# Performance work log

Measured on AMD Instinct MI355X. Metric: run time of the kernel, lower is better.

Reference implementation:

```python
import math
import jax, jax.numpy as jnp
import numpy as np

N_HEAD = 16

def _slopes(n_head):
    # Matches MHA_aLiBi.get_slope (static, so computed with numpy)
    cp2 = 2 ** int(math.floor(math.log2(n_head)))
    slopes = (0.5) ** np.arange(1, cp2 + 1)
    if cp2 < n_head:
        intra = 1.0 / math.sqrt(2.0)
        pair = intra ** np.arange(1, 1 + 2 * (n_head - cp2), 2)
        slopes = np.sort(np.concatenate([slopes, pair]))[::-1]
    return jnp.asarray(slopes, dtype=jnp.float32)  # [H]

def _alibi_bias(S):
    # bias[i,j] = -(i-j) for i>=j, 0 for i<j
    d = jnp.arange(S)[:, None] - jnp.arange(S)[None, :]
    return -jnp.maximum(d, 0).astype(jnp.float32)  # [S,S]

def setup_inputs() -> dict:
    key = jax.random.key(0)
    B, S, D = 2, 2048, 1024
    ks = jax.random.split(key, 12)
    f = lambda k, sh: jax.random.normal(k, sh, dtype=jnp.float32)
    inp = {
        "q": f(ks[0], (B, S, D)),
        "k": f(ks[1], (B, S, D)),
        "v": f(ks[2], (B, S, D)),
        "mask": jnp.tril(jnp.ones((S, S), dtype=jnp.int32))[None, None],  # causal [1,1,S,S]
        "wq_w": f(ks[3], (D, D)) * 0.02, "wq_b": f(ks[4], (D,)) * 0.02,
        "wk_w": f(ks[5], (D, D)) * 0.02, "wk_b": f(ks[6], (D,)) * 0.02,
        "wv_w": f(ks[7], (D, D)) * 0.02, "wv_b": f(ks[8], (D,)) * 0.02,
        "out_w": f(ks[9], (D, D)) * 0.02, "out_b": f(ks[10], (D,)) * 0.02,
    }
    return inp

def reference(q, k, v, mask, wq_w, wq_b, wk_w, wk_b, wv_w, wv_b, out_w, out_b):
    B, S, D = q.shape
    H = N_HEAD
    hd = D // H
    lin = lambda x, w, b: x @ w.T + b  # torch nn.Linear
    # project and split heads: [B,S,D] -> [B,H,S,hd]
    split = lambda x: x.reshape(B, S, H, hd).transpose(0, 2, 1, 3)
    wq = split(lin(q, wq_w, wq_b))
    wk = split(lin(k, wk_w, wk_b))
    wv = split(lin(v, wv_w, wv_b))
    qk = jnp.einsum("bhsd,bhtd->bhst", wq, wk)  # [B,H,S,S] (no 1/sqrt(d) scaling, per source)
    alibi = _alibi_bias(S)[None, :, :] * _slopes(H)[:, None, None]  # [H,S,S]
    attn = qk + alibi[None]
    attn = jnp.where(mask == 0, jnp.float32(-1e9), attn)
    attn = jax.nn.softmax(attn, axis=-1)
    out = jnp.einsum("bhst,bhtd->bhsd", attn, wv)
    out = out.transpose(0, 2, 1, 3).reshape(B, S, D)
    return lin(out, out_w, out_b)
```

## Files before the change

kernel.cpp:

```cpp
#include <hip/hip_runtime.h>
#include <hip/hip_bf16.h>
#include <cstdint>
#include <cstddef>

#define DEV static __device__ __forceinline__

typedef float f32x4 __attribute__((ext_vector_type(4)));
typedef __bf16 bf16x8 __attribute__((ext_vector_type(8)));
typedef __bf16 bf16x4 __attribute__((ext_vector_type(4)));

#define EXP2F(x) __builtin_amdgcn_exp2f(x)

union B8 {
  uint4 u4;
  uint32_t u[4];
  unsigned short s[8];
  bf16x8 v;
};
union B4 {
  uint2 u2;
  unsigned short s[4];
  bf16x4 v;
};

DEV unsigned short bfbits(float x) {
  union { __bf16 h; unsigned short s; } z; z.h = (__bf16)x; return z.s;
}
DEV uint32_t pk2(float x, float y) {
  union { __bf16 h[2]; uint32_t u; } z;
  z.h[0] = (__bf16)x; z.h[1] = (__bf16)y; return z.u;
}

DEV f32x4 mfma_bf16(bf16x8 a, bf16x8 b, f32x4 c) {
  return __builtin_amdgcn_mfma_f32_16x16x32_bf16(a, b, c, 0, 0, 0);
}

DEV void gload16(const void* g, void* l) {
  __builtin_amdgcn_global_load_lds(
      (const __attribute__((address_space(1))) void*)g,
      (__attribute__((address_space(3))) void*)l, 16, 0, 0);
}

__global__ __launch_bounds__(256)
void cvt_all(const float* __restrict__ q, const float* __restrict__ k,
             const float* __restrict__ v,
             const float* __restrict__ wq, const float* __restrict__ wk,
             const float* __restrict__ wv, const float* __restrict__ ow,
             unsigned short* __restrict__ dst) {
  const int bid = blockIdx.x;
  const size_t base = ((size_t)bid << 11) + ((size_t)threadIdx.x << 3);
  const float* src;
  size_t rel;
  if (bid < 2048)      { src = q; rel = base; }
  else if (bid < 4096) { src = k; rel = base - (1u << 22); }
  else if (bid < 6144) { src = v; rel = base - (2u << 22); }
  else {
    const int wseg = (bid - 6144) >> 9;
    src = wseg == 0 ? wq : wseg == 1 ? wk : wseg == 2 ? wv : ow;
    rel = base & 1048575u;
  }
  float4 a0 = *(const float4*)(src + rel);
  float4 a1 = *(const float4*)(src + rel + 4);
  B8 p;
  p.u[0] = pk2(a0.x, a0.y); p.u[1] = pk2(a0.z, a0.w);
  p.u[2] = pk2(a1.x, a1.y); p.u[3] = pk2(a1.z, a1.w);
  *(uint4*)(dst + base) = p.u4;
}

__global__ __launch_bounds__(256, 2)
void gemm_qkv_b(const unsigned short* __restrict__ qb,
                const unsigned short* __restrict__ kb,
                const unsigned short* __restrict__ vb,
                const unsigned short* __restrict__ wqb,
                const unsigned short* __restrict__ wkb,
                const unsigned short* __restrict__ wvb,
                const float* __restrict__ bq, const float* __restrict__ bk,
                const float* __restrict__ bv,
                unsigned short* __restrict__ Qp, unsigned short* __restrict__ Kp,
                unsigned short* __restrict__ Vt) {
  const int K = 1024, N = 1024;
  __shared__ __align__(16) unsigned short As[64 * 64];
  __shared__ __align__(16) unsigned short Bs[128 * 64];
  const int bid = blockIdx.x;
  const int lbid = (bid & 7) * 192 + (bid >> 3);
  const int proj = lbid >> 9;
  const int t = lbid & 511;
  const int mb = t >> 3, nb = t & 7;
  const unsigned short* A  = proj == 0 ? qb  : proj == 1 ? kb  : vb;
  const unsigned short* Bw = proj == 0 ? wqb : proj == 1 ? wkb : wvb;
  const float* bias        = proj == 0 ? bq  : proj == 1 ? bk  : bv;
  const int tid = threadIdx.x;
  const int lane = tid & 63, w = tid >> 6;
  const int qc = lane & 15, g = lane >> 4;
  f32x4 acc[4][2] = {};

  const int lrow = lane >> 3, lg = lane & 7;
  const int gsrc = lg ^ lrow;
  const unsigned short* ag = A  + (size_t)(mb * 64 + w * 16 + lrow) * K + gsrc * 8;
  const unsigned short* bg = Bw + (size_t)(nb * 128 + w * 32 + lrow) * K + gsrc * 8;
  unsigned short* al = &As[(w * 16) * 64];
  unsigned short* bl = &Bs[(w * 32) * 64];

  for (int kt = 0; kt < 16; ++kt) {
    __syncthreads();
#pragma unroll
    for (int i = 0; i < 2; ++i)
      gload16(ag + i * (8 * 1024) + kt * 64, al + (i * 8) * 64);
#pragma unroll
    for (int i = 0; i < 4; ++i)
      gload16(bg + i * (8 * 1024) + kt * 64, bl + (i * 8) * 64);
    __syncthreads();

    B8 af[4][2], bfr[2][2];
#pragma unroll
    for (int mi = 0; mi < 4; ++mi)
#pragma unroll
      for (int kk = 0; kk < 2; ++kk) {
        const int row = mi * 16 + qc;
        const int slot = ((kk << 2) + g) ^ (row & 7);
        af[mi][kk].u4 = *(const uint4*)&As[(row << 6) + (slot << 3)];
      }
#pragma unroll
    for (int ni = 0; ni < 2; ++ni)
#pragma unroll
      for (int kk = 0; kk < 2; ++kk) {
        const int row = w * 32 + ni * 16 + qc;
        const int slot = ((kk << 2) + g) ^ (row & 7);
        bfr[ni][kk].u4 = *(const uint4*)&Bs[(row << 6) + (slot << 3)];
      }
#pragma unroll
    for (int kk = 0; kk < 2; ++kk)
#pragma unroll
      for (int mi = 0; mi < 4; ++mi)
#pragma unroll
        for (int ni = 0; ni < 2; ++ni)
          acc[mi][ni] = mfma_bf16(af[mi][kk].v, bfr[ni][kk].v, acc[mi][ni]);
  }

  unsigned short* Cv = proj == 0 ? Qp : proj == 1 ? Kp : Vt;
  const bool vt_mode = (proj == 2);
#pragma unroll
  for (int ni = 0; ni < 2; ++ni) {
    const int col = nb * 128 + w * 32 + ni * 16 + qc;
    const float bv = bias[col];
#pragma unroll
    for (int mi = 0; mi < 4; ++mi) {
#pragma unroll
      for (int r = 0; r < 4; ++r) {
        const int row = mb * 64 + mi * 16 + g * 4 + r;
        const float val = acc[mi][ni][r] + bv;
        if (!vt_mode) {
          Cv[(size_t)row * N + col] = bfbits(val);
        } else {
          const int b = row >> 11, ss = row & 2047, hh = col >> 6, d = col & 63;
          Cv[((size_t)((b * 16 + hh) * 64 + d) << 11) + ss] = bfbits(val);
        }
      }
    }
  }
}

__global__ __launch_bounds__(256, 2)
void gemm_out_b(const unsigned short* __restrict__ At,
                const unsigned short* __restrict__ wob,
                const float* __restrict__ bias, float* __restrict__ Cv) {
  const int K = 1024, N = 1024;
  __shared__ __align__(16) unsigned short As[64 * 64];
  __shared__ __align__(16) unsigned short Bs[128 * 64];
  const int bid = blockIdx.x;
  const int lbid = (bid & 7) * 64 + (bid >> 3);
  const int mb = lbid >> 3, nb = lbid & 7;
  const int tid = threadIdx.x;
  const int lane = tid & 63, w = tid >> 6;
  const int qc = lane & 15, g = lane >> 4;
  f32x4 acc[4][2] = {};

  const int lrow = lane >> 3, lg = lane & 7;
  const int gsrc = lg ^ lrow;
  const unsigned short* ag = At  + (size_t)(mb * 64 + w * 16 + lrow) * K + gsrc * 8;
  const unsigned short* bg = wob + (size_t)(nb * 128 + w * 32 + lrow) * K + gsrc * 8;
  unsigned short* al = &As[(w * 16) * 64];
  unsigned short* bl = &Bs[(w * 32) * 64];

  for (int kt = 0; kt < 16; ++kt) {
    __syncthreads();
#pragma unroll
    for (int i = 0; i < 2; ++i)
      gload16(ag + i * (8 * 1024) + kt * 64, al + (i * 8) * 64);
#pragma unroll
    for (int i = 0; i < 4; ++i)
      gload16(bg + i * (8 * 1024) + kt * 64, bl + (i * 8) * 64);
    __syncthreads();

    B8 af[4][2], bfr[2][2];
#pragma unroll
    for (int mi = 0; mi < 4; ++mi)
#pragma unroll
      for (int kk = 0; kk < 2; ++kk) {
        const int row = mi * 16 + qc;
        const int slot = ((kk << 2) + g) ^ (row & 7);
        af[mi][kk].u4 = *(const uint4*)&As[(row << 6) + (slot << 3)];
      }
#pragma unroll
    for (int ni = 0; ni < 2; ++ni)
#pragma unroll
      for (int kk = 0; kk < 2; ++kk) {
        const int row = w * 32 + ni * 16 + qc;
        const int slot = ((kk << 2) + g) ^ (row & 7);
        bfr[ni][kk].u4 = *(const uint4*)&Bs[(row << 6) + (slot << 3)];
      }
#pragma unroll
    for (int kk = 0; kk < 2; ++kk)
#pragma unroll
      for (int mi = 0; mi < 4; ++mi)
#pragma unroll
        for (int ni = 0; ni < 2; ++ni)
          acc[mi][ni] = mfma_bf16(af[mi][kk].v, bfr[ni][kk].v, acc[mi][ni]);
  }

#pragma unroll
  for (int ni = 0; ni < 2; ++ni) {
    const int col = nb * 128 + w * 32 + ni * 16 + qc;
    const float bv = bias[col];
#pragma unroll
    for (int mi = 0; mi < 4; ++mi) {
#pragma unroll
      for (int r = 0; r < 4; ++r) {
        const int row = mb * 64 + mi * 16 + g * 4 + r;
        Cv[(size_t)row * N + col] = acc[mi][ni][r] + bv;
      }
    }
  }
}

__global__ __launch_bounds__(256, 4)
void flash_alibi(const unsigned short* __restrict__ Qp,
                 const unsigned short* __restrict__ Kp,
                 const unsigned short* __restrict__ Vt,
                 unsigned short* __restrict__ At) {
  const int S = 2048, Dm = 1024;
  const int bid0 = blockIdx.x;
  const int lbid = (bid0 & 7) * 128 + (bid0 >> 3);
  const int z = lbid >> 5, y = lbid & 31;
  const int s = ((8 * (y & 3)) + (y >> 2) + 8 * (z & 3) + (z >> 2)) & 31;
  const int h = z & 15, b = z >> 4;
  const int tid = threadIdx.x, lane = tid & 63, w = tid >> 6;
  const int qc = lane & 15, g = lane >> 4;
  const int q0 = s * 64 + w * 16;
  const int qcol = q0 + qc;
  const float slope = exp2f(-(float)(h + 1));
  const float L2E = 1.44269504f;
  const float ls1 = L2E * slope;
  const float THR = 11.54f;
  const size_t bS = (size_t)b * S;
  const int hoff = h * 64;
  const int ntile = s + 1;

  __shared__ __align__(16) unsigned short Ks[64 * 64];
  __shared__ __align__(16) unsigned short Vs[64 * 64];

  B8 qf[2];
  {
    const unsigned short* qa = Qp + (bS + qcol) * Dm + hoff + g * 8;
    qf[0].u4 = *(const uint4*)qa; qf[1].u4 = *(const uint4*)(qa + 32);
  }

  const int q7 = qc & 7;
  const int gk0 = g ^ q7;
  const int gk1 = gk0 ^ 4;
  const int krow = w * 16 + qc;
  const unsigned short* kgA = Kp + (bS + krow) * Dm + hoff + g * 8;
  const unsigned short* kgB = Kp + (bS + krow) * Dm + hoff + (g ^ 4) * 8;
  const unsigned short* vgA =
      Vt + (((size_t)((b * 16 + h) * 64 + krow)) << 11) + g * 8;
  const unsigned short* vgB =
      Vt + (((size_t)((b * 16 + h) * 64 + krow)) << 11) + (g ^ 4) * 8;
  unsigned short* kwA = &Ks[krow * 64 + gk0 * 8];
  unsigned short* kwB = &Ks[krow * 64 + gk1 * 8];
  unsigned short* vwA = &Vs[krow * 64 + gk0 * 8];
  unsigned short* vwB = &Vs[krow * 64 + gk1 * 8];
  uint4 krA, krB, vrA, vrB;

#define SLOAD(TT) do {                                                         \
    const size_t ko_ = ((size_t)(TT) << 6) * Dm;                               \
    krA = *(const uint4*)(kgA + ko_); krB = *(const uint4*)(kgB + ko_);        \
    vrA = *(const uint4*)(vgA + ((TT) << 6));                                  \
    vrB = *(const uint4*)(vgB + ((TT) << 6));                                  \
  } while (0)
#define SWRITE() do {                                                          \
    *(uint4*)kwA = krA; *(uint4*)kwB = krB;                                    \
    *(uint4*)vwA = vrA; *(uint4*)vwB = vrB;                                    \
  } while (0)

  const int sw = qc & 7;
  const unsigned short* krd0 = &Ks[qc * 64 + ((g ^ sw) << 3)];
  const unsigned short* krd1 = &Ks[qc * 64 + (((g ^ sw) ^ 4) << 3)];
  const unsigned short* vrd[4];
#pragma unroll
  for (int j = 0; j < 4; ++j)
    vrd[j] = &Vs[qc * 64 + ((((2 * j) + (g >> 1)) ^ sw) << 3) + (g & 1) * 4];

  f32x4 acc[4] = {};
  float m_run = 0.f, l_run = 0.f;
  const float abq = slope * (float)(g * 4 - qcol);

#define FRAGX(KV0, MASKED) do {                                                \
    const float kv0f = (float)(KV0);                                           \
    f32x4 sc_[4] = {};                                                         \
    _Pragma("unroll")                                                          \
    for (int f_ = 0; f_ < 4; ++f_) {                                           \
      B8 k0_, k1_;                                                             \
      k0_.u4 = *(const uint4*)(krd0 + f_ * 1024);                              \
      k1_.u4 = *(const uint4*)(krd1 + f_ * 1024);                              \
      sc_[f_] = mfma_bf16(k0_.v, qf[0].v, sc_[f_]);                            \
      sc_[f_] = mfma_bf16(k1_.v, qf[1].v, sc_[f_]);                            \
    }                                                                          \
    const float cb_ = (fmaf(slope, kv0f, abq) - m_run) * L2E;                  \
    float ein_[4][4]; float emax_ = -1e30f;                                    \
    _Pragma("unroll")                                                          \
    for (int f_ = 0; f_ < 4; ++f_) {                                           \
      const float cf_ = cb_ + (float)(16 * f_) * ls1;                          \
      _Pragma("unroll")                                                        \
      for (int r_ = 0; r_ < 4; ++r_) {                                         \
        float e_ = fmaf(sc_[f_][r_], L2E, cf_ + (float)r_ * ls1);              \
        if (MASKED) {                                                          \
          const int kv_ = (KV0) + f_ * 16 + g * 4 + r_;                        \
          if (kv_ > qcol) e_ = -1e30f;                                         \
        }                                                                      \
        ein_[f_][r_] = e_; emax_ = fmaxf(emax_, e_);                           \
      }                                                                        \
    }                                                                          \
    if (!__all(emax_ <= THR)) {                                                \
      float er_ = fmaxf(emax_, __shfl_xor(emax_, 16));                         \
      er_ = fmaxf(er_, __shfl_xor(er_, 32));                                   \
      er_ = fmaxf(er_, 0.f);                                                   \
      m_run += er_ * 0.69314718f;                                              \
      const float sfac_ = EXP2F(-er_);                                         \
      l_run *= sfac_;                                                          \
      _Pragma("unroll") for (int n_ = 0; n_ < 4; ++n_) acc[n_] = acc[n_] * sfac_; \
      _Pragma("unroll") for (int f_ = 0; f_ < 4; ++f_)                         \
        _Pragma("unroll") for (int r_ = 0; r_ < 4; ++r_) ein_[f_][r_] -= er_;  \
    }                                                                          \
    B8 pf0_, pf1_; float lsum_ = 0.f;                                          \
    _Pragma("unroll")                                                          \
    for (int f_ = 0; f_ < 4; ++f_) {                                           \
      _Pragma("unroll")                                                        \
      for (int r_ = 0; r_ < 4; ++r_) {                                         \
        const float p_ = EXP2F(ein_[f_][r_]);                                  \
        lsum_ += p_;                                                           \
        if (f_ == 0)      pf0_.v[r_]     = (__bf16)p_;                         \
        else if (f_ == 1) pf0_.v[4 + r_] = (__bf16)p_;                         \
        else if (f_ == 2) pf1_.v[r_]     = (__bf16)p_;                         \
        else              pf1_.v[4 + r_] = (__bf16)p_;                         \
      }                                                                        \
    }                                                                          \
    l_run += lsum_;                                                            \
    _Pragma("unroll")                                                          \
    for (int n_ = 0; n_ < 4; ++n_) {                                           \
      B8 v0_, v1_;                                                             \
      uint2 a0_ = *(const uint2*)(vrd[0] + n_ * 1024);                         \
      uint2 a1_ = *(const uint2*)(vrd[1] + n_ * 1024);                         \
      uint2 a2_ = *(const uint2*)(vrd[2] + n_ * 1024);                         \
      uint2 a3_ = *(const uint2*)(vrd[3] + n_ * 1024);                         \
      v0_.u[0] = a0_.x; v0_.u[1] = a0_.y;                                      \
      v0_.u[2] = a1_.x; v0_.u[3] = a1_.y;                                      \
      v1_.u[0] = a2_.x; v1_.u[1] = a2_.y;                                      \
      v1_.u[2] = a3_.x; v1_.u[3] = a3_.y;                                      \
      acc[n_] = mfma_bf16(v0_.v, pf0_.v, acc[n_]);                             \
      acc[n_] = mfma_bf16(v1_.v, pf1_.v, acc[n_]);                             \
    }                                                                          \
  } while (0)

  SLOAD(0);
  SWRITE();
  __syncthreads();

  for (int t = 0; t < ntile - 1; ++t) {
    SLOAD(t + 1);
    FRAGX(t << 6, 0);
    __syncthreads();
    SWRITE();
    __syncthreads();
  }
  FRAGX((ntile - 1) << 6, 1);

  float lt = l_run + __shfl_xor(l_run, 16);
  lt += __shfl_xor(lt, 32);
  const float ri = 1.0f / lt;
  unsigned short* ob = At + (bS + qcol) * Dm + hoff;
#pragma unroll
  for (int n = 0; n < 4; ++n) {
    B4 ov;
    ov.v[0] = (__bf16)(acc[n][0] * ri);
    ov.v[1] = (__bf16)(acc[n][1] * ri);
    ov.v[2] = (__bf16)(acc[n][2] * ri);
    ov.v[3] = (__bf16)(acc[n][3] * ri);
    *(uint2*)(ob + n * 16 + g * 4) = ov.u2;
  }
}

extern "C" void kernel_launch(void* const* d_in, const int* in_sizes, int n_in,
                              void* d_out, int out_size, void* d_ws, size_t ws_size,
                              hipStream_t stream) {
  const float* q    = (const float*)d_in[0];
  const float* k    = (const float*)d_in[1];
  const float* v    = (const float*)d_in[2];
  const float* wq_w = (const float*)d_in[4];
  const float* wq_b = (const float*)d_in[5];
  const float* wk_w = (const float*)d_in[6];
  const float* wk_b = (const float*)d_in[7];
  const float* wv_w = (const float*)d_in[8];
  const float* wv_b = (const float*)d_in[9];
  const float* ow   = (const float*)d_in[10];
  const float* ob   = (const float*)d_in[11];
  float* out = (float*)d_out;

  char* ws = (char*)d_ws;
  unsigned short* Qp = (unsigned short*)(ws);
  unsigned short* Kp = (unsigned short*)(ws + (8u << 20));
  unsigned short* Vt = (unsigned short*)(ws + (16u << 20));
  unsigned short* At = (unsigned short*)(ws + (24u << 20));
  unsigned short* cvt = (unsigned short*)(ws + (32u << 20));
  unsigned short* qb  = cvt;
  unsigned short* kb  = cvt + (1u << 22);
  unsigned short* vb  = cvt + (2u << 22);
  unsigned short* wqb = cvt + (3u << 22);
  unsigned short* wkb = wqb + (1u << 20);
  unsigned short* wvb = wkb + (1u << 20);
  unsigned short* wob = wvb + (1u << 20);

  dim3 blk(256);
  cvt_all<<<8192, blk, 0, stream>>>(q, k, v, wq_w, wk_w, wv_w, ow, cvt);
  gemm_qkv_b<<<1536, blk, 0, stream>>>(qb, kb, vb, wqb, wkb, wvb,
                                       wq_b, wk_b, wv_b, Qp, Kp, Vt);
  flash_alibi<<<1024, blk, 0, stream>>>(Qp, Kp, Vt, At);
  gemm_out_b<<<512, blk, 0, stream>>>(At, wob, ob, out);
}
```

Baseline: 127.1 us.

## Double-buffer shared memory in QKV GEMM and attention kernels

Both the QKV projection GEMM and the attention kernel now use two shared-memory buffers. The next tile is staged into the spare buffer while the current one is computed, which cuts each iteration's two barriers down to one. The intent is to overlap global-to-LDS transfer with MFMA work and reduce synchronisation stalls. The cost is double the LDS footprint, which may lower occupancy.

```diff
diff --git a/kernel.cpp b/kernel.cpp
--- a/kernel.cpp
+++ b/kernel.cpp
@@ -79,8 +79,8 @@
                 unsigned short* __restrict__ Qp, unsigned short* __restrict__ Kp,
                 unsigned short* __restrict__ Vt) {
   const int K = 1024, N = 1024;
-  __shared__ __align__(16) unsigned short As[64 * 64];
-  __shared__ __align__(16) unsigned short Bs[128 * 64];
+  __shared__ __align__(16) unsigned short As[2][64 * 64];
+  __shared__ __align__(16) unsigned short Bs[2][128 * 64];
   const int bid = blockIdx.x;
   const int lbid = (bid & 7) * 192 + (bid >> 3);
   const int proj = lbid >> 9;
@@ -98,18 +98,22 @@
   const int gsrc = lg ^ lrow;
   const unsigned short* ag = A  + (size_t)(mb * 64 + w * 16 + lrow) * K + gsrc * 8;
   const unsigned short* bg = Bw + (size_t)(nb * 128 + w * 32 + lrow) * K + gsrc * 8;
-  unsigned short* al = &As[(w * 16) * 64];
-  unsigned short* bl = &Bs[(w * 32) * 64];
+
+#define QSTAGE(BB, KT) do {                                                    \
+    _Pragma("unroll")                                                          \
+    for (int i_ = 0; i_ < 2; ++i_)                                             \
+      gload16(ag + i_ * (8 * 1024) + (KT) * 64, &As[BB][(w * 16 + i_ * 8) * 64]); \
+    _Pragma("unroll")                                                          \
+    for (int i_ = 0; i_ < 4; ++i_)                                             \
+      gload16(bg + i_ * (8 * 1024) + (KT) * 64, &Bs[BB][(w * 32 + i_ * 8) * 64]); \
+  } while (0)
+
+  QSTAGE(0, 0);
+  __syncthreads();
 
   for (int kt = 0; kt < 16; ++kt) {
-    __syncthreads();
-#pragma unroll
-    for (int i = 0; i < 2; ++i)
-      gload16(ag + i * (8 * 1024) + kt * 64, al + (i * 8) * 64);
-#pragma unroll
-    for (int i = 0; i < 4; ++i)
-      gload16(bg + i * (8 * 1024) + kt * 64, bl + (i * 8) * 64);
-    __syncthreads();
+    const int cur = kt & 1;
+    if (kt < 15) QSTAGE(cur ^ 1, kt + 1);
 
     B8 af[4][2], bfr[2][2];
 #pragma unroll
@@ -118,7 +122,7 @@
       for (int kk = 0; kk < 2; ++kk) {
         const int row = mi * 16 + qc;
         const int slot = ((kk << 2) + g) ^ (row & 7);
-        af[mi][kk].u4 = *(const uint4*)&As[(row << 6) + (slot << 3)];
+        af[mi][kk].u4 = *(const uint4*)&As[cur][(row << 6) + (slot << 3)];
       }
 #pragma unroll
     for (int ni = 0; ni < 2; ++ni)
@@ -126,7 +130,7 @@
       for (int kk = 0; kk < 2; ++kk) {
         const int row = w * 32 + ni * 16 + qc;
         const int slot = ((kk << 2) + g) ^ (row & 7);
-        bfr[ni][kk].u4 = *(const uint4*)&Bs[(row << 6) + (slot << 3)];
+        bfr[ni][kk].u4 = *(const uint4*)&Bs[cur][(row << 6) + (slot << 3)];
       }
 #pragma unroll
     for (int kk = 0; kk < 2; ++kk)
@@ -135,6 +139,8 @@
 #pragma unroll
         for (int ni = 0; ni < 2; ++ni)
           acc[mi][ni] = mfma_bf16(af[mi][kk].v, bfr[ni][kk].v, acc[mi][ni]);
+
+    __syncthreads();
   }
 
   unsigned short* Cv = proj == 0 ? Qp : proj == 1 ? Kp : Vt;
@@ -256,8 +262,8 @@
   const int hoff = h * 64;
   const int ntile = s + 1;
 
-  __shared__ __align__(16) unsigned short Ks[64 * 64];
-  __shared__ __align__(16) unsigned short Vs[64 * 64];
+  __shared__ __align__(16) unsigned short Ks[2][64 * 64];
+  __shared__ __align__(16) unsigned short Vs[2][64 * 64];
 
   B8 qf[2];
   {
@@ -275,10 +281,10 @@
       Vt + (((size_t)((b * 16 + h) * 64 + krow)) << 11) + g * 8;
   const unsigned short* vgB =
       Vt + (((size_t)((b * 16 + h) * 64 + krow)) << 11) + (g ^ 4) * 8;
-  unsigned short* kwA = &Ks[krow * 64 + gk0 * 8];
-  unsigned short* kwB = &Ks[krow * 64 + gk1 * 8];
-  unsigned short* vwA = &Vs[krow * 64 + gk0 * 8];
-  unsigned short* vwB = &Vs[krow * 64 + gk1 * 8];
+  unsigned short* kwA = &Ks[0][krow * 64 + gk0 * 8];
+  unsigned short* kwB = &Ks[0][krow * 64 + gk1 * 8];
+  unsigned short* vwA = &Vs[0][krow * 64 + gk0 * 8];
+  unsigned short* vwB = &Vs[0][krow * 64 + gk1 * 8];
   uint4 krA, krB, vrA, vrB;
 
 #define SLOAD(TT) do {                                                         \
@@ -287,31 +293,31 @@
     vrA = *(const uint4*)(vgA + ((TT) << 6));                                  \
     vrB = *(const uint4*)(vgB + ((TT) << 6));                                  \
   } while (0)
-#define SWRITE() do {                                                          \
-    *(uint4*)kwA = krA; *(uint4*)kwB = krB;                                    \
-    *(uint4*)vwA = vrA; *(uint4*)vwB = vrB;                                    \
+#define SWRITE(BO) do {                                                        \
+    *(uint4*)(kwA + (BO)) = krA; *(uint4*)(kwB + (BO)) = krB;                  \
+    *(uint4*)(vwA + (BO)) = vrA; *(uint4*)(vwB + (BO)) = vrB;                  \
   } while (0)
 
   const int sw = qc & 7;
-  const unsigned short* krd0 = &Ks[qc * 64 + ((g ^ sw) << 3)];
-  const unsigned short* krd1 = &Ks[qc * 64 + (((g ^ sw) ^ 4) << 3)];
+  const unsigned short* krd0 = &Ks[0][qc * 64 + ((g ^ sw) << 3)];
+  const unsigned short* krd1 = &Ks[0][qc * 64 + (((g ^ sw) ^ 4) << 3)];
   const unsigned short* vrd[4];
 #pragma unroll
   for (int j = 0; j < 4; ++j)
-    vrd[j] = &Vs[qc * 64 + ((((2 * j) + (g >> 1)) ^ sw) << 3) + (g & 1) * 4];
+    vrd[j] = &Vs[0][qc * 64 + ((((2 * j) + (g >> 1)) ^ sw) << 3) + (g & 1) * 4];
 
   f32x4 acc[4] = {};
   float m_run = 0.f, l_run = 0.f;
   const float abq = slope * (float)(g * 4 - qcol);
 
-#define FRAGX(KV0, MASKED) do {                                                \
+#define FRAGX(KV0, BO, MASKED) do {                                            \
     const float kv0f = (float)(KV0);                                           \
     f32x4 sc_[4] = {};                                                         \
     _Pragma("unroll")                                                          \
     for (int f_ = 0; f_ < 4; ++f_) {                                           \
       B8 k0_, k1_;                                                             \
-      k0_.u4 = *(const uint4*)(krd0 + f_ * 1024);                              \
-      k1_.u4 = *(const uint4*)(krd1 + f_ * 1024);                              \
+      k0_.u4 = *(const uint4*)(krd0 + (BO) + f_ * 1024);                       \
+      k1_.u4 = *(const uint4*)(krd1 + (BO) + f_ * 1024);                       \
       sc_[f_] = mfma_bf16(k0_.v, qf[0].v, sc_[f_]);                            \
       sc_[f_] = mfma_bf16(k1_.v, qf[1].v, sc_[f_]);                            \
     }                                                                          \
@@ -358,10 +364,10 @@
     _Pragma("unroll")                                                          \
     for (int n_ = 0; n_ < 4; ++n_) {                                           \
       B8 v0_, v1_;                                                             \
-      uint2 a0_ = *(const uint2*)(vrd[0] + n_ * 1024);                         \
-      uint2 a1_ = *(const uint2*)(vrd[1] + n_ * 1024);                         \
-      uint2 a2_ = *(const uint2*)(vrd[2] + n_ * 1024);                         \
-      uint2 a3_ = *(const uint2*)(vrd[3] + n_ * 1024);                         \
+      uint2 a0_ = *(const uint2*)(vrd[0] + (BO) + n_ * 1024);                  \
+      uint2 a1_ = *(const uint2*)(vrd[1] + (BO) + n_ * 1024);                  \
+      uint2 a2_ = *(const uint2*)(vrd[2] + (BO) + n_ * 1024);                  \
+      uint2 a3_ = *(const uint2*)(vrd[3] + (BO) + n_ * 1024);                  \
       v0_.u[0] = a0_.x; v0_.u[1] = a0_.y;                                      \
       v0_.u[2] = a1_.x; v0_.u[3] = a1_.y;                                      \
       v1_.u[0] = a2_.x; v1_.u[1] = a2_.y;                                      \
@@ -372,17 +378,17 @@
   } while (0)
 
   SLOAD(0);
-  SWRITE();
+  SWRITE(0);
   __syncthreads();
 
   for (int t = 0; t < ntile - 1; ++t) {
+    const int bo = (t & 1) << 12;
     SLOAD(t + 1);
-    FRAGX(t << 6, 0);
+    FRAGX(t << 6, bo, 0);
+    SWRITE(bo ^ 4096);
     __syncthreads();
-    SWRITE();
-    __syncthreads();
-  }
-  FRAGX((ntile - 1) << 6, 1);
+  }
+  FRAGX((ntile - 1) << 6, ((ntile - 1) & 1) << 12, 1);
 
   float lt = l_run + __shfl_xor(l_run, 16);
   lt += __shfl_xor(lt, 32);
```

New measurement: 134.4 us. 5.7% more time.
